# Kernel optimization log

Hardware: AMD Instinct MI355X
Metric: run time of the kernel (lower is better)

The kernel has to match this reference:

```python
import jax, jax.numpy as jnp
import numpy as np

B, N, E, H, Z = 8, 10000, 160000, 128, 64

def setup_inputs() -> dict:
    key = jax.random.key(0)
    ks = jax.random.split(key, 12)
    def w(k, shape):
        fan_in = shape[-1]
        return (jax.random.uniform(k, shape, jnp.float32, -1.0, 1.0) / np.sqrt(fan_in)).astype(jnp.float32)
    return {
        "x_node": jax.random.normal(ks[0], (B, N), jnp.float32),
        "edge_index": jax.random.randint(ks[1], (2, E), 0, N, dtype=jnp.int64),
        # layer 1: SAGEConv(1 -> H)
        "W1l": w(ks[2], (H, 1)), "b1": jnp.zeros((H,), jnp.float32), "W1r": w(ks[3], (H, 1)),
        # layer 2: SAGEConv(H -> H)
        "W2l": w(ks[4], (H, H)), "b2": jnp.zeros((H,), jnp.float32), "W2r": w(ks[5], (H, H)),
        # readout MLP: Linear(H,H) -> ReLU -> Linear(H,Z)
        "Wro1": w(ks[6], (H, H)), "bro1": jnp.zeros((H,), jnp.float32),
        "Wro2": w(ks[7], (Z, H)), "bro2": jnp.zeros((Z,), jnp.float32),
    }

def _sage_conv(h, src, dst, n_nodes, Wl, bl, Wr):
    """h: (B, N, din). out_i = Wl @ mean_{j->i} h_j + bl + Wr @ h_i."""
    msg = h[:, src, :]  # (B, E, din) gather from source nodes
    agg_sum = jax.vmap(lambda m: jax.ops.segment_sum(m, dst, num_segments=n_nodes))(msg)  # (B, N, din)
    deg = jax.ops.segment_sum(jnp.ones(dst.shape, h.dtype), dst, num_segments=n_nodes)  # (N,)
    agg = agg_sum / jnp.maximum(deg, 1.0)[None, :, None]  # mean; 0 for isolated nodes
    return jnp.einsum('bnd,hd->bnh', agg, Wl) + bl + jnp.einsum('bnd,hd->bnh', h, Wr)

def reference(x_node, edge_index, W1l, b1, W1r, W2l, b2, W2r, Wro1, bro1, Wro2, bro2):
    bsz, n = x_node.shape
    src, dst = edge_index[0], edge_index[1]
    h = x_node[:, :, None]  # (B, N, 1)
    h = jax.nn.relu(_sage_conv(h, src, dst, n, W1l, b1, W1r))
    h = jax.nn.relu(_sage_conv(h, src, dst, n, W2l, b2, W2r))
    pooled = jnp.mean(h, axis=1)  # global_mean_pool over nodes -> (B, H)
    hid = jax.nn.relu(pooled @ Wro1.T + bro1)
    return hid @ Wro2.T + bro2  # (B, Z)
```

## Files before the change

kernel.cpp:

```cpp
#include <hip/hip_runtime.h>
#include <hip/hip_bf16.h>

#define Bk 8
#define Nk 10000
#define Ek 160000
#define Hk 128
#define Zk 64
#define CAPk 64
#define NTILES 313
#define NROWS 10016

typedef float f32x4 __attribute__((ext_vector_type(4)));
typedef float f32x2 __attribute__((ext_vector_type(2)));
typedef short s16x8 __attribute__((ext_vector_type(8)));

__device__ inline f32x2 pk_add(f32x2 a, f32x2 b){
  f32x2 d; asm("v_pk_add_f32 %0, %1, %2" : "=v"(d) : "v"(a), "v"(b)); return d;
}
__device__ inline f32x2 bf2_to_f32x2(unsigned v){
  f32x2 r; r.x = __uint_as_float(v<<16); r.y = __uint_as_float(v & 0xffff0000u); return r;
}
__device__ inline unsigned pack_bf2(float lo, float hi){
  __hip_bfloat162 p; p.x = __float2bfloat16(lo); p.y = __float2bfloat16(hi);
  return *(unsigned*)&p;
}

__global__ __launch_bounds__(256) void k0_init(const float* __restrict__ W2l, const float* __restrict__ W2r,
                                               __hip_bfloat16* __restrict__ wbt, int* __restrict__ cur,
                                               float* __restrict__ pooled){
  int t = blockIdx.x*256 + threadIdx.x;
  if (t < 128*256){
    int o = t >> 8, k = t & 255;
    float v = (k < 128) ? W2l[o*128+k] : W2r[o*128+(k-128)];
    wbt[t] = __float2bfloat16(v);
  }
  if (t < Nk) cur[t] = 0;
  if (t < Bk*Hk) pooled[t] = 0.f;
}

__global__ void k3_fill(const int* __restrict__ ei, int* __restrict__ cur, int* __restrict__ csrsrc){
  int e = blockIdx.x*blockDim.x + threadIdx.x;
  if (e < Ek){
    int s = ei[e], d = ei[Ek+e];
    int p = atomicAdd(&cur[d], 1);
    if (p < CAPk) csrsrc[d*CAPk + p] = s;
  }
}

__global__ __launch_bounds__(256) void k45_h1(const float* __restrict__ x, const int* __restrict__ cur,
                        int* __restrict__ csrsrc,
                        const float* __restrict__ W1l, const float* __restrict__ b1,
                        const float* __restrict__ W1r, __hip_bfloat16* __restrict__ h1){
  int i = blockIdx.x*4 + (threadIdx.x>>6);
  int lane = threadIdx.x & 63;
  if (i >= Nk){
    if (i < NROWS){
      #pragma unroll
      for (int b=0;b<Bk;b++)
        *(unsigned*)((void*)(h1 + ((size_t)b*NROWS + i)*128 + 2*lane)) = 0u;
    }
    return;
  }
  float2 wl = *(const float2*)(W1l + 2*lane);
  float2 wr = *(const float2*)(W1r + 2*lane);
  float2 bb = *(const float2*)(b1  + 2*lane);
  int degc = cur[i];
  int deg = min(degc, CAPk);
  int deg4 = (deg + 3) & ~3;
  int* col = csrsrc + (size_t)i*CAPk;
  int j = 0;
  bool havej = (lane < deg);
  if (havej) j = col[lane];
  if (lane >= deg && lane < deg4) col[lane] = Nk;
  float inv = 1.f/fmaxf((float)degc, 1.f);

  float xx[Bk];
  #pragma unroll
  for (int b=0;b<Bk;b++){
    float v = 0.f;
    if (havej) v = x[b*Nk + j];
    xx[b] = v;
  }
  #pragma unroll
  for (int b=0;b<Bk;b++){
    float s = xx[b];
    s += __shfl_xor(s, 1);  s += __shfl_xor(s, 2);  s += __shfl_xor(s, 4);
    s += __shfl_xor(s, 8);  s += __shfl_xor(s, 16); s += __shfl_xor(s, 32);
    float a  = s * inv;
    float xi = x[b*Nk + i];
    float v0 = fmaxf(fmaf(a, wl.x, fmaf(xi, wr.x, bb.x)), 0.f);
    float v1 = fmaxf(fmaf(a, wl.y, fmaf(xi, wr.y, bb.y)), 0.f);
    *(unsigned*)((void*)(h1 + ((size_t)b*NROWS + i)*128 + 2*lane)) = pack_bf2(v0, v1);
  }
}

__device__ inline void mfma_bf16(f32x4& d, s16x8 a, s16x8 b){
  asm("v_mfma_f32_16x16x32_bf16 %0, %1, %2, %0" : "+v"(d) : "v"(a), "v"(b));
}

__global__ __launch_bounds__(256) void kB_fused(const __hip_bfloat16* __restrict__ h1,
                        const int* __restrict__ cur, const int* __restrict__ csrsrc,
                        const __hip_bfloat16* __restrict__ wbt, const float* __restrict__ b2,
                        float* __restrict__ pooled){
  __shared__ char At[32*512];
  int b = blockIdx.x, tile = blockIdx.y;
  int wid = threadIdx.x >> 6, lane = threadIdx.x & 63;
  int g = lane >> 4, l4 = lane & 15;
  const __hip_bfloat16* h1b = h1 + (size_t)b*NROWS*128;

  for (int c=0;c<8;c++){
    int r = wid*8 + c;
    int i = tile*32 + r;
    f32x2 acc0 = {0.f,0.f}, acc1 = {0.f,0.f}, acc2 = {0.f,0.f}, acc3 = {0.f,0.f};
    float inv = 0.f;
    if (i < Nk){
      int degc = cur[i];
      int deg = min(degc, CAPk);
      int deg4 = (deg + 3) & ~3;
      const int* col = csrsrc + (size_t)i*CAPk;
      #pragma unroll 2
      for (int k4=0; k4<deg4; k4+=4){
        int j = col[k4 + g];
        uint4 v = *(const uint4*)((const void*)(h1b + (size_t)j*128 + l4*8));
        acc0 = pk_add(acc0, bf2_to_f32x2(v.x));
        acc1 = pk_add(acc1, bf2_to_f32x2(v.y));
        acc2 = pk_add(acc2, bf2_to_f32x2(v.z));
        acc3 = pk_add(acc3, bf2_to_f32x2(v.w));
      }
      inv = 1.f/fmaxf((float)degc, 1.f);
    }
    #pragma unroll
    for (int m=16; m<=32; m<<=1){
      acc0.x += __shfl_xor(acc0.x, m); acc0.y += __shfl_xor(acc0.y, m);
      acc1.x += __shfl_xor(acc1.x, m); acc1.y += __shfl_xor(acc1.y, m);
      acc2.x += __shfl_xor(acc2.x, m); acc2.y += __shfl_xor(acc2.y, m);
      acc3.x += __shfl_xor(acc3.x, m); acc3.y += __shfl_xor(acc3.y, m);
    }
    unsigned swz = (unsigned)((r & 7) << 4);
    if (g == 0){
      uint4 outv;
      outv.x = pack_bf2(acc0.x*inv, acc0.y*inv);
      outv.y = pack_bf2(acc1.x*inv, acc1.y*inv);
      outv.z = pack_bf2(acc2.x*inv, acc2.y*inv);
      outv.w = pack_bf2(acc3.x*inv, acc3.y*inv);
      *(uint4*)(At + r*512 + ((unsigned)(l4*16) ^ swz)) = outv;
    } else if (g == 1){
      uint4 sv = *(const uint4*)((const void*)(h1b + (size_t)i*128 + l4*8));
      *(uint4*)(At + r*512 + ((unsigned)(256 + l4*16) ^ swz)) = sv;
    }
  }
  __syncthreads();

  int lr = lane & 15, lk = lane >> 4;
  f32x4 acc[2][2];
  #pragma unroll
  for (int mf=0; mf<2; ++mf)
    #pragma unroll
    for (int q=0; q<2; ++q) acc[mf][q] = (f32x4){0.f,0.f,0.f,0.f};

  unsigned rsw = (unsigned)((lr & 7) << 4);
  #pragma unroll
  for (int kk=0; kk<8; ++kk){
    unsigned cb = kk*64 + lk*16;
    s16x8 a0 = *(const s16x8*)(At + lr*512      + (cb ^ rsw));
    s16x8 a1 = *(const s16x8*)(At + (16+lr)*512 + (cb ^ rsw));
    #pragma unroll
    for (int q=0; q<2; ++q){
      int nf = wid*2 + q;
      s16x8 bfr = *(const s16x8*)(const void*)(wbt + (nf*16+lr)*256 + kk*32 + lk*8);
      mfma_bf16(acc[0][q], a0, bfr);
      mfma_bf16(acc[1][q], a1, bfr);
    }
  }

  #pragma unroll
  for (int q=0; q<2; ++q){
    int colc = (wid*2+q)*16 + lr;
    float bias = b2[colc];
    float v = 0.f;
    #pragma unroll
    for (int mf=0; mf<2; ++mf){
      int rbase = tile*32 + mf*16 + lk*4;
      #pragma unroll
      for (int r=0;r<4;++r){
        float val = fmaxf(acc[mf][q][r] + bias, 0.f);
        if (rbase + r < Nk) v += val;
      }
    }
    v += __shfl_xor(v, 16);
    v += __shfl_xor(v, 32);
    if (lane < 16) atomicAdd(&pooled[b*Hk + colc], v);
  }
}

__global__ void k7_final(const float* __restrict__ pooled, const float* __restrict__ Wro1,
                         const float* __restrict__ bro1, const float* __restrict__ Wro2,
                         const float* __restrict__ bro2, float* __restrict__ out){
  int b = blockIdx.x, t = threadIdx.x;
  __shared__ float pool[128];
  __shared__ float hid[128];
  pool[t] = pooled[b*Hk + t] * (1.0f/(float)Nk);
  __syncthreads();
  float s = bro1[t];
  for (int d=0; d<128; ++d) s += Wro1[t*128+d]*pool[d];
  hid[t] = fmaxf(s, 0.f);
  __syncthreads();
  if (t < Zk){
    float s2 = bro2[t];
    for (int d=0; d<128; ++d) s2 += Wro2[t*128+d]*hid[d];
    out[b*Zk + t] = s2;
  }
}

extern "C" void kernel_launch(void* const* d_in, const int* in_sizes, int n_in,
                              void* d_out, int out_size, void* d_ws, size_t ws_size,
                              hipStream_t stream) {
  const float* x    = (const float*)d_in[0];
  const int*   ei   = (const int*)d_in[1];
  const float* W1l  = (const float*)d_in[2];
  const float* b1   = (const float*)d_in[3];
  const float* W1r  = (const float*)d_in[4];
  const float* W2l  = (const float*)d_in[5];
  const float* b2   = (const float*)d_in[6];
  const float* W2r  = (const float*)d_in[7];
  const float* Wro1 = (const float*)d_in[8];
  const float* bro1 = (const float*)d_in[9];
  const float* Wro2 = (const float*)d_in[10];
  const float* bro2 = (const float*)d_in[11];
  float* out = (float*)d_out;

  char* ws = (char*)d_ws;
  int*   cur    = (int*)(ws + 0);
  float* pooled = (float*)(ws + 40448);
  __hip_bfloat16* wbt = (__hip_bfloat16*)(ws + 44544);
  int*   csrsrc = (int*)(ws + 110080);
  __hip_bfloat16* h1 = (__hip_bfloat16*)(ws + 2670080);

  k0_init<<<dim3(128), 256, 0, stream>>>(W2l, W2r, wbt, cur, pooled);
  k3_fill<<<dim3((Ek+255)/256), 256, 0, stream>>>(ei, cur, csrsrc);
  k45_h1<<<dim3(2504), 256, 0, stream>>>(x, cur, csrsrc, W1l, b1, W1r, h1);
  kB_fused<<<dim3(Bk, NTILES), 256, 0, stream>>>(h1, cur, csrsrc, wbt, b2, pooled);
  k7_final<<<dim3(Bk), 128, 0, stream>>>(pooled, Wro1, bro1, Wro2, bro2, out);
}
```

Baseline: 108.7 us.

## Stage CSR columns in LDS and interleave two rows' gathers per wave

```diff
diff --git a/kernel.cpp b/kernel.cpp
--- a/kernel.cpp
+++ b/kernel.cpp
@@ -13,6 +13,7 @@
 typedef float f32x4 __attribute__((ext_vector_type(4)));
 typedef float f32x2 __attribute__((ext_vector_type(2)));
 typedef short s16x8 __attribute__((ext_vector_type(8)));
+typedef unsigned u32x4 __attribute__((ext_vector_type(4)));
 
 __device__ inline f32x2 pk_add(f32x2 a, f32x2 b){
   f32x2 d; asm("v_pk_add_f32 %0, %1, %2" : "=v"(d) : "v"(a), "v"(b)); return d;
@@ -103,50 +104,90 @@
                         const __hip_bfloat16* __restrict__ wbt, const float* __restrict__ b2,
                         float* __restrict__ pooled){
   __shared__ char At[32*512];
+  __shared__ int scol[32*CAPk];
+  __shared__ int sdeg[32];
   int b = blockIdx.x, tile = blockIdx.y;
-  int wid = threadIdx.x >> 6, lane = threadIdx.x & 63;
+  int tid = threadIdx.x;
+  int wid = tid >> 6, lane = tid & 63;
   int g = lane >> 4, l4 = lane & 15;
   const __hip_bfloat16* h1b = h1 + (size_t)b*NROWS*128;
 
-  for (int c=0;c<8;c++){
-    int r = wid*8 + c;
-    int i = tile*32 + r;
-    f32x2 acc0 = {0.f,0.f}, acc1 = {0.f,0.f}, acc2 = {0.f,0.f}, acc3 = {0.f,0.f};
-    float inv = 0.f;
-    if (i < Nk){
-      int degc = cur[i];
-      int deg = min(degc, CAPk);
-      int deg4 = (deg + 3) & ~3;
-      const int* col = csrsrc + (size_t)i*CAPk;
-      #pragma unroll 2
-      for (int k4=0; k4<deg4; k4+=4){
-        int j = col[k4 + g];
-        uint4 v = *(const uint4*)((const void*)(h1b + (size_t)j*128 + l4*8));
-        acc0 = pk_add(acc0, bf2_to_f32x2(v.x));
-        acc1 = pk_add(acc1, bf2_to_f32x2(v.y));
-        acc2 = pk_add(acc2, bf2_to_f32x2(v.z));
-        acc3 = pk_add(acc3, bf2_to_f32x2(v.w));
+  {
+    const u32x4* src = (const u32x4*)(csrsrc + (size_t)tile*32*CAPk);
+    u32x4* dst = (u32x4*)scol;
+    dst[tid]       = __builtin_nontemporal_load(src + tid);
+    dst[256 + tid] = __builtin_nontemporal_load(src + 256 + tid);
+    if (tid < 32){
+      int i = tile*32 + tid;
+      sdeg[tid] = (i < Nk) ? cur[i] : 0;
+    }
+  }
+  __syncthreads();
+
+  for (int c=0;c<4;c++){
+    int rA = wid*8 + 2*c, rB = rA + 1;
+    int iA = tile*32 + rA, iB = iA + 1;
+    int dcA = sdeg[rA], dcB = sdeg[rB];
+    int d4A = (min(dcA,CAPk)+3)&~3, d4B = (min(dcB,CAPk)+3)&~3;
+
+    u32x4 svA = {0,0,0,0}, svB = {0,0,0,0};
+    if (g == 1) svA = *(const u32x4*)((const void*)(h1b + (size_t)iA*128 + l4*8));
+    if (g == 3) svB = *(const u32x4*)((const void*)(h1b + (size_t)iB*128 + l4*8));
+
+    f32x2 aA0={0.f,0.f}, aA1={0.f,0.f}, aA2={0.f,0.f}, aA3={0.f,0.f};
+    f32x2 aB0={0.f,0.f}, aB1={0.f,0.f}, aB2={0.f,0.f}, aB3={0.f,0.f};
+    int mx = max(d4A, d4B);
+    for (int k4=0; k4<mx; k4+=4){
+      if (k4 < d4A){
+        int j = scol[rA*CAPk + k4 + g];
+        u32x4 v = *(const u32x4*)((const void*)(h1b + (size_t)j*128 + l4*8));
+        aA0 = pk_add(aA0, bf2_to_f32x2(v.x));
+        aA1 = pk_add(aA1, bf2_to_f32x2(v.y));
+        aA2 = pk_add(aA2, bf2_to_f32x2(v.z));
+        aA3 = pk_add(aA3, bf2_to_f32x2(v.w));
       }
-      inv = 1.f/fmaxf((float)degc, 1.f);
+      if (k4 < d4B){
+        int j = scol[rB*CAPk + k4 + g];
+        u32x4 v = *(const u32x4*)((const void*)(h1b + (size_t)j*128 + l4*8));
+        aB0 = pk_add(aB0, bf2_to_f32x2(v.x));
+        aB1 = pk_add(aB1, bf2_to_f32x2(v.y));
+        aB2 = pk_add(aB2, bf2_to_f32x2(v.z));
+        aB3 = pk_add(aB3, bf2_to_f32x2(v.w));
+      }
     }
     #pragma unroll
     for (int m=16; m<=32; m<<=1){
-      acc0.x += __shfl_xor(acc0.x, m); acc0.y += __shfl_xor(acc0.y, m);
-      acc1.x += __shfl_xor(acc1.x, m); acc1.y += __shfl_xor(acc1.y, m);
-      acc2.x += __shfl_xor(acc2.x, m); acc2.y += __shfl_xor(acc2.y, m);
-      acc3.x += __shfl_xor(acc3.x, m); acc3.y += __shfl_xor(acc3.y, m);
-    }
-    unsigned swz = (unsigned)((r & 7) << 4);
+      aA0.x += __shfl_xor(aA0.x, m); aA0.y += __shfl_xor(aA0.y, m);
+      aA1.x += __shfl_xor(aA1.x, m); aA1.y += __shfl_xor(aA1.y, m);
+      aA2.x += __shfl_xor(aA2.x, m); aA2.y += __shfl_xor(aA2.y, m);
+      aA3.x += __shfl_xor(aA3.x, m); aA3.y += __shfl_xor(aA3.y, m);
+      aB0.x += __shfl_xor(aB0.x, m); aB0.y += __shfl_xor(aB0.y, m);
+      aB1.x += __shfl_xor(aB1.x, m); aB1.y += __shfl_xor(aB1.y, m);
+      aB2.x += __shfl_xor(aB2.x, m); aB2.y += __shfl_xor(aB2.y, m);
+      aB3.x += __shfl_xor(aB3.x, m); aB3.y += __shfl_xor(aB3.y, m);
+    }
+    float invA = 1.f/fmaxf((float)dcA, 1.f);
+    float invB = 1.f/fmaxf((float)dcB, 1.f);
+    unsigned swzA = (unsigned)((rA & 7) << 4);
+    unsigned swzB = (unsigned)((rB & 7) << 4);
     if (g == 0){
-      uint4 outv;
-      outv.x = pack_bf2(acc0.x*inv, acc0.y*inv);
-      outv.y = pack_bf2(acc1.x*inv, acc1.y*inv);
-      outv.z = pack_bf2(acc2.x*inv, acc2.y*inv);
-      outv.w = pack_bf2(acc3.x*inv, acc3.y*inv);
-      *(uint4*)(At + r*512 + ((unsigned)(l4*16) ^ swz)) = outv;
+      u32x4 outv;
+      outv.x = pack_bf2(aA0.x*invA, aA0.y*invA);
+      outv.y = pack_bf2(aA1.x*invA, aA1.y*invA);
+      outv.z = pack_bf2(aA2.x*invA, aA2.y*invA);
+      outv.w = pack_bf2(aA3.x*invA, aA3.y*invA);
+      *(u32x4*)(At + rA*512 + ((unsigned)(l4*16) ^ swzA)) = outv;
     } else if (g == 1){
-      uint4 sv = *(const uint4*)((const void*)(h1b + (size_t)i*128 + l4*8));
-      *(uint4*)(At + r*512 + ((unsigned)(256 + l4*16) ^ swz)) = sv;
+      *(u32x4*)(At + rA*512 + ((unsigned)(256 + l4*16) ^ swzA)) = svA;
+    } else if (g == 2){
+      u32x4 outv;
+      outv.x = pack_bf2(aB0.x*invB, aB0.y*invB);
+      outv.y = pack_bf2(aB1.x*invB, aB1.y*invB);
+      outv.z = pack_bf2(aB2.x*invB, aB2.y*invB);
+      outv.w = pack_bf2(aB3.x*invB, aB3.y*invB);
+      *(u32x4*)(At + rB*512 + ((unsigned)(l4*16) ^ swzB)) = outv;
+    } else {
+      *(u32x4*)(At + rB*512 + ((unsigned)(256 + l4*16) ^ swzB)) = svB;
     }
   }
   __syncthreads();
@@ -234,7 +275,7 @@
   float* pooled = (float*)(ws + 40448);
   __hip_bfloat16* wbt = (__hip_bfloat16*)(ws + 44544);
   int*   csrsrc = (int*)(ws + 110080);
-  __hip_bfloat16* h1 = (__hip_bfloat16*)(ws + 2670080);
+  __hip_bfloat16* h1 = (__hip_bfloat16*)(ws + 2674176);
 
   k0_init<<<dim3(128), 256, 0, stream>>>(W2l, W2r, wbt, cur, pooled);
   k3_fill<<<dim3((Ek+255)/256), 256, 0, stream>>>(ei, cur, csrsrc);
```

New measurement: 101.2 us. 1.07x faster.

## Stage CSR neighbor lists in LDS and gather one row per 16-lane group

Applied to the files above, without the earlier changes.

```diff
diff --git a/kernel.cpp b/kernel.cpp
--- a/kernel.cpp
+++ b/kernel.cpp
@@ -13,6 +13,7 @@
 typedef float f32x4 __attribute__((ext_vector_type(4)));
 typedef float f32x2 __attribute__((ext_vector_type(2)));
 typedef short s16x8 __attribute__((ext_vector_type(8)));
+typedef unsigned u32x4 __attribute__((ext_vector_type(4)));
 
 __device__ inline f32x2 pk_add(f32x2 a, f32x2 b){
   f32x2 d; asm("v_pk_add_f32 %0, %1, %2" : "=v"(d) : "v"(a), "v"(b)); return d;
@@ -48,7 +49,7 @@
 }
 
 __global__ __launch_bounds__(256) void k45_h1(const float* __restrict__ x, const int* __restrict__ cur,
-                        int* __restrict__ csrsrc,
+                        const int* __restrict__ csrsrc,
                         const float* __restrict__ W1l, const float* __restrict__ b1,
                         const float* __restrict__ W1r, __hip_bfloat16* __restrict__ h1){
   int i = blockIdx.x*4 + (threadIdx.x>>6);
@@ -66,12 +67,10 @@
   float2 bb = *(const float2*)(b1  + 2*lane);
   int degc = cur[i];
   int deg = min(degc, CAPk);
-  int deg4 = (deg + 3) & ~3;
-  int* col = csrsrc + (size_t)i*CAPk;
+  const int* col = csrsrc + (size_t)i*CAPk;
   int j = 0;
   bool havej = (lane < deg);
   if (havej) j = col[lane];
-  if (lane >= deg && lane < deg4) col[lane] = Nk;
   float inv = 1.f/fmaxf((float)degc, 1.f);
 
   float xx[Bk];
@@ -103,51 +102,71 @@
                         const __hip_bfloat16* __restrict__ wbt, const float* __restrict__ b2,
                         float* __restrict__ pooled){
   __shared__ char At[32*512];
+  __shared__ int scol[32*CAPk];
+  __shared__ int sdeg[32];
   int b = blockIdx.x, tile = blockIdx.y;
-  int wid = threadIdx.x >> 6, lane = threadIdx.x & 63;
+  int tid = threadIdx.x;
+  int wid = tid >> 6, lane = tid & 63;
   int g = lane >> 4, l4 = lane & 15;
   const __hip_bfloat16* h1b = h1 + (size_t)b*NROWS*128;
 
-  for (int c=0;c<8;c++){
-    int r = wid*8 + c;
-    int i = tile*32 + r;
-    f32x2 acc0 = {0.f,0.f}, acc1 = {0.f,0.f}, acc2 = {0.f,0.f}, acc3 = {0.f,0.f};
-    float inv = 0.f;
-    if (i < Nk){
-      int degc = cur[i];
-      int deg = min(degc, CAPk);
-      int deg4 = (deg + 3) & ~3;
-      const int* col = csrsrc + (size_t)i*CAPk;
-      #pragma unroll 2
-      for (int k4=0; k4<deg4; k4+=4){
-        int j = col[k4 + g];
-        uint4 v = *(const uint4*)((const void*)(h1b + (size_t)j*128 + l4*8));
-        acc0 = pk_add(acc0, bf2_to_f32x2(v.x));
-        acc1 = pk_add(acc1, bf2_to_f32x2(v.y));
-        acc2 = pk_add(acc2, bf2_to_f32x2(v.z));
-        acc3 = pk_add(acc3, bf2_to_f32x2(v.w));
-      }
-      inv = 1.f/fmaxf((float)degc, 1.f);
-    }
-    #pragma unroll
-    for (int m=16; m<=32; m<<=1){
-      acc0.x += __shfl_xor(acc0.x, m); acc0.y += __shfl_xor(acc0.y, m);
-      acc1.x += __shfl_xor(acc1.x, m); acc1.y += __shfl_xor(acc1.y, m);
-      acc2.x += __shfl_xor(acc2.x, m); acc2.y += __shfl_xor(acc2.y, m);
-      acc3.x += __shfl_xor(acc3.x, m); acc3.y += __shfl_xor(acc3.y, m);
-    }
-    unsigned swz = (unsigned)((r & 7) << 4);
-    if (g == 0){
-      uint4 outv;
-      outv.x = pack_bf2(acc0.x*inv, acc0.y*inv);
-      outv.y = pack_bf2(acc1.x*inv, acc1.y*inv);
-      outv.z = pack_bf2(acc2.x*inv, acc2.y*inv);
-      outv.w = pack_bf2(acc3.x*inv, acc3.y*inv);
-      *(uint4*)(At + r*512 + ((unsigned)(l4*16) ^ swz)) = outv;
-    } else if (g == 1){
-      uint4 sv = *(const uint4*)((const void*)(h1b + (size_t)i*128 + l4*8));
-      *(uint4*)(At + r*512 + ((unsigned)(256 + l4*16) ^ swz)) = sv;
-    }
+  if (tid < 32){
+    int i = tile*32 + tid;
+    sdeg[tid] = (i < Nk) ? cur[i] : 0;
+  }
+  __syncthreads();
+
+  {
+    const u32x4* src = (const u32x4*)(csrsrc + (size_t)tile*32*CAPk);
+    u32x4* dst = (u32x4*)scol;
+    #pragma unroll
+    for (int h=0; h<2; ++h){
+      int idx = h*256 + tid;
+      u32x4 v = __builtin_nontemporal_load(src + idx);
+      int row = idx >> 4;
+      int p = (idx & 15) * 4;
+      int d = min(sdeg[row], CAPk);
+      if (p+0 >= d) v.x = Nk;
+      if (p+1 >= d) v.y = Nk;
+      if (p+2 >= d) v.z = Nk;
+      if (p+3 >= d) v.w = Nk;
+      dst[idx] = v;
+    }
+  }
+  __syncthreads();
+
+  #pragma unroll
+  for (int c=0;c<2;c++){
+    int rg = wid*8 + c*4 + g;
+    int ig = tile*32 + rg;
+    int dc = sdeg[rg];
+    int d4 = (min(dc, CAPk) + 3) & ~3;
+    int km = d4;
+    km = max(km, __shfl_xor(km, 16));
+    km = max(km, __shfl_xor(km, 32));
+
+    u32x4 sv = *(const u32x4*)((const void*)(h1b + (size_t)ig*128 + l4*8));
+
+    f32x2 a0={0.f,0.f}, a1={0.f,0.f}, a2={0.f,0.f}, a3={0.f,0.f};
+    const int* colg = scol + rg*CAPk;
+    #pragma unroll 2
+    for (int k=0; k<km; ++k){
+      int j = colg[k];
+      u32x4 v = *(const u32x4*)((const void*)(h1b + (size_t)j*128 + l4*8));
+      a0 = pk_add(a0, bf2_to_f32x2(v.x));
+      a1 = pk_add(a1, bf2_to_f32x2(v.y));
+      a2 = pk_add(a2, bf2_to_f32x2(v.z));
+      a3 = pk_add(a3, bf2_to_f32x2(v.w));
+    }
+    float inv = 1.f/fmaxf((float)dc, 1.f);
+    u32x4 outv;
+    outv.x = pack_bf2(a0.x*inv, a0.y*inv);
+    outv.y = pack_bf2(a1.x*inv, a1.y*inv);
+    outv.z = pack_bf2(a2.x*inv, a2.y*inv);
+    outv.w = pack_bf2(a3.x*inv, a3.y*inv);
+    unsigned swz = (unsigned)((rg & 7) << 4);
+    *(u32x4*)(At + rg*512 + ((unsigned)(l4*16) ^ swz))       = outv;
+    *(u32x4*)(At + rg*512 + ((unsigned)(256 + l4*16) ^ swz)) = sv;
   }
   __syncthreads();
 
@@ -234,7 +253,7 @@
   float* pooled = (float*)(ws + 40448);
   __hip_bfloat16* wbt = (__hip_bfloat16*)(ws + 44544);
   int*   csrsrc = (int*)(ws + 110080);
-  __hip_bfloat16* h1 = (__hip_bfloat16*)(ws + 2670080);
+  __hip_bfloat16* h1 = (__hip_bfloat16*)(ws + 2674176);
 
   k0_init<<<dim3(128), 256, 0, stream>>>(W2l, W2r, wbt, cur, pooled);
   k3_fill<<<dim3((Ek+255)/256), 256, 0, stream>>>(ei, cur, csrsrc);
```

Result: faster. 96.24 us (-11.4%).
